# Optimization experiments

Measured on AMD Instinct MI355X. Metric: run time of the kernel, lower is better.

Reference implementation:

```python
import jax, jax.numpy as jnp
import numpy as np
from jax import lax

BATCH = 524288
N_LINKS = 8   # body 0 = fixed base, bodies 1..7 have revolute joints
N_DOFS = 7
G = 9.81      # base linear acceleration z-component encodes gravity

def _skew(v):
    x, y, z = v[..., 0], v[..., 1], v[..., 2]
    o = jnp.zeros_like(x)
    return jnp.stack([jnp.stack([o, -z, y], -1),
                      jnp.stack([z, o, -x], -1),
                      jnp.stack([-y, x, o], -1)], -2)

def _rodrigues(axis, theta):
    # rotation about unit axis by theta; broadcasts axis[...,3] with theta[...]
    K = _skew(axis)
    s = jnp.sin(theta)[..., None, None]
    c = jnp.cos(theta)[..., None, None]
    I = jnp.eye(3, dtype=jnp.result_type(theta))
    return I + s * K + (1.0 - c) * (K @ K)

def setup_inputs():
    key = jax.random.key(0)
    ks = jax.random.split(key, 10)
    q = jax.random.normal(ks[0], (BATCH, N_DOFS), jnp.float32)
    qd = jax.random.normal(ks[1], (BATCH, N_DOFS), jnp.float32)
    qdd_des = jax.random.normal(ks[2], (BATCH, N_DOFS), jnp.float32)
    # fixed (URDF) joint transforms: valid random rotations + link-offset translations
    ax = jax.random.normal(ks[3], (N_LINKS, 3), jnp.float32)
    ax = ax / jnp.linalg.norm(ax, axis=-1, keepdims=True)
    ang = jax.random.uniform(ks[4], (N_LINKS,), jnp.float32, -1.0, 1.0)
    rot_fix = _rodrigues(ax, ang)
    trans_fix = jax.random.uniform(ks[5], (N_LINKS, 3), jnp.float32, -0.25, 0.25)
    # single-coordinate joint axes with signs, as in URDF revolute joints
    joint_axes = jnp.asarray([[0, 0, 1], [0, 1, 0], [0, 0, 1], [0, -1, 0],
                              [0, 0, 1], [0, 1, 0], [0, 0, 1]], jnp.float32)
    mass = jax.random.uniform(ks[6], (N_LINKS,), jnp.float32, 0.5, 4.0)
    com = 0.05 * jax.random.normal(ks[7], (N_LINKS, 3), jnp.float32)
    A = 0.1 * jax.random.normal(ks[8], (N_LINKS, 3, 3), jnp.float32)
    inertia = A @ jnp.swapaxes(A, -1, -2) + 0.05 * jnp.eye(3, dtype=jnp.float32)
    damping = jax.random.uniform(ks[9], (N_DOFS,), jnp.float32, 0.01, 0.2)
    return dict(q=q, qd=qd, qdd_des=qdd_des, rot_fix=rot_fix, trans_fix=trans_fix,
                joint_axes=joint_axes, mass=mass, com=com, inertia=inertia, damping=damping)

def reference(q, qd, qdd_des, rot_fix, trans_fix, joint_axes, mass, com, inertia, damping):
    # Batched recursive Newton-Euler inverse dynamics over a serial chain,
    # matching DifferentiableRobotModel.compute_inverse_dynamics (gravity+damping on).
    B, D = q.shape
    # joint pose of body i(=dof j+1): rotation = rot_fix[i] @ R(axis_j, q_j), translation = trans_fix[i]
    Rq = _rodrigues(joint_axes[None, :, :], q)                     # [B,D,3,3]
    R = jnp.einsum('dij,bdjk->dbik', rot_fix[1:], Rq)              # [D,B,3,3]
    p = trans_fix[1:]                                              # [D,3]
    jv = qd.T[:, :, None] * joint_axes[:, None, :]                 # [D,B,3] joint angular vel
    ja = qdd_des.T[:, :, None] * joint_axes[:, None, :]            # [D,B,3] joint angular acc

    z = jnp.zeros((B, 3), q.dtype)
    base_acc_lin = z.at[:, 2].set(G)

    # forward pass: propagate spatial velocity/acceleration root -> leaf
    def fwd_step(carry, xs):
        vl, va, al, aa = carry
        Ri, pi, jvi, jai = xs
        Rt = jnp.swapaxes(Ri, -1, -2)
        pinv = -jnp.einsum('bij,j->bi', Rt, pi)
        # SpatialMotionVec.transform with inverse joint pose (Rt, pinv)
        va_n = jnp.einsum('bij,bj->bi', Rt, va)
        vl_n = jnp.einsum('bij,bj->bi', Rt, vl) + jnp.cross(pinv, va_n)
        va_i = va_n + jvi
        vl_i = vl_n
        aa_n = jnp.einsum('bij,bj->bi', Rt, aa)
        al_n = jnp.einsum('bij,bj->bi', Rt, al) + jnp.cross(pinv, aa_n)
        # acc = parent_acc(transformed) + joint_acc + vel x joint_vel (joint_vel.lin = 0)
        aa_i = aa_n + jai + jnp.cross(va_i, jvi)
        al_i = al_n + jnp.cross(vl_i, jvi)
        new = (vl_i, va_i, al_i, aa_i)
        return new, new

    _, (vl, va, al, aa) = lax.scan(fwd_step, (z, z, base_acc_lin, z), (R, p, jv, ja))

    # spatial inertia (about body frame origin) acting on motion vectors
    m = mass[1:, None, None]                                       # [D,1,1]
    mc = mass[1:, None] * com[1:]                                  # [D,3]
    cs = _skew(com[1:])
    Io = inertia[1:] + mass[1:, None, None] * (cs @ jnp.swapaxes(cs, -1, -2))

    def imul(lin, ang):
        return (m * lin + jnp.cross(ang, mc[:, None, :]),
                jnp.einsum('dij,dbj->dbi', Io, ang) + jnp.cross(mc[:, None, :], lin))

    Ia_l, Ia_a = imul(al, aa)
    Iv_l, Iv_a = imul(vl, va)
    # f = I*acc + vel x* (I*vel)
    f_l = Ia_l + jnp.cross(va, Iv_l)
    f_a = Ia_a + jnp.cross(va, Iv_a) + jnp.cross(vl, Iv_l)

    # backward pass: accumulate forces leaf -> root; tau_j = f.ang . axis_j
    def bwd_step(carry, xs):
        cl, ca = carry
        fl, fa, Ri, pi, axi = xs
        tl = fl + cl
        ta = fa + ca
        tau = jnp.einsum('bi,i->b', ta, axi)
        # SpatialForceVec.transform with joint pose (Ri, pi)
        nl = jnp.einsum('bij,bj->bi', Ri, tl)
        na = jnp.einsum('bij,bj->bi', Ri, ta) + jnp.cross(pi[None, :], nl)
        return (nl, na), tau

    _, taus = lax.scan(bwd_step, (z, z), (f_l, f_a, R, p, joint_axes), reverse=True)
    return jnp.swapaxes(taus, 0, 1) + damping[None, :] * qd        # [B,D]
```

## Files before the change

kernel.cpp:

```cpp
#include <hip/hip_runtime.h>

#define NDOF 7
#define BLK 256
#define CST_STRIDE 24
#define CST_TOT (NDOF * CST_STRIDE)
#define SF_FLOATS (NDOF * 6 * BLK)

struct V3 { float x, y, z; };
__device__ __forceinline__ V3 operator+(V3 a, V3 b) { return {a.x + b.x, a.y + b.y, a.z + b.z}; }
__device__ __forceinline__ V3 operator-(V3 a, V3 b) { return {a.x - b.x, a.y - b.y, a.z - b.z}; }
__device__ __forceinline__ V3 operator*(float s, V3 a) { return {s * a.x, s * a.y, s * a.z}; }
__device__ __forceinline__ V3 cross(V3 a, V3 b) {
    return {a.y * b.z - a.z * b.y, a.z * b.x - a.x * b.z, a.x * b.y - a.y * b.x};
}
__device__ __forceinline__ float dot(V3 a, V3 b) { return a.x * b.x + a.y * b.y + a.z * b.z; }

template <int AX>
__device__ __forceinline__ void make_R(V3 Fc0, V3 Fc1, V3 Fc2, float s, float c,
                                       V3& R0, V3& R1, V3& R2) {
    if (AX == 0) {
        R0 = c * Fc0 + s * Fc1;
        R1 = c * Fc1 - s * Fc0;
        R2 = Fc2;
    } else if (AX == 1) {
        R0 = c * Fc0 - s * Fc2;
        R1 = Fc1;
        R2 = s * Fc0 + c * Fc2;
    } else {
        R0 = c * Fc0 + s * Fc2;
        R1 = Fc1;
        R2 = c * Fc2 - s * Fc0;
    }
}

template <int AX>
__device__ __forceinline__ void fwd_step(const float4* C4, float s, float c,
                                         float qd, float qdd, V3& vl, V3& va, V3& al,
                                         V3& aa, V3& fl, V3& fa) {
    const float4 A0 = C4[0], A1 = C4[1], A2 = C4[2], A3 = C4[3], A4 = C4[4], A5 = C4[5];
    const V3 Fc0{A0.x, A0.y, A0.z};
    const V3 Fc1{A0.w, A1.x, A1.y};
    const V3 Fc2{A1.z, A1.w, A2.x};
    const V3 p{A2.y, A2.z, A2.w};
    const float I00 = A3.x, I01 = A3.y, I02 = A3.z, I11 = A3.w, I12 = A4.x, I22 = A4.y;
    const float m = A4.z;
    const V3 mc{A4.w, A5.x, A5.y};

    V3 R0, R1, R2;
    make_R<AX>(Fc0, Fc1, Fc2, s, c, R0, R1, R2);

    V3 w1 = vl + cross(va, p);
    V3 w2 = al + cross(aa, p);
    V3 nvl{dot(R0, w1), dot(R1, w1), dot(R2, w1)};
    V3 nva{dot(R0, va), dot(R1, va), dot(R2, va)};
    V3 nal{dot(R0, w2), dot(R1, w2), dot(R2, w2)};
    V3 naa{dot(R0, aa), dot(R1, aa), dot(R2, aa)};

    if (AX == 0) {
        va = {nva.x, nva.y, nva.z + qd};
        aa = {naa.x + va.y * qd, naa.y - va.x * qd, naa.z + qdd};
        vl = nvl;
        al = {nal.x + vl.y * qd, nal.y - vl.x * qd, nal.z};
    } else if (AX == 1) {
        va = {nva.x, nva.y + qd, nva.z};
        aa = {naa.x - va.z * qd, naa.y + qdd, naa.z + va.x * qd};
        vl = nvl;
        al = {nal.x - vl.z * qd, nal.y, nal.z + vl.x * qd};
    } else {
        va = {nva.x, nva.y - qd, nva.z};
        aa = {naa.x + va.z * qd, naa.y - qdd, naa.z - va.x * qd};
        vl = nvl;
        al = {nal.x + vl.z * qd, nal.y, nal.z - vl.x * qd};
    }

    V3 Ial = m * al + cross(aa, mc);
    V3 Iaa = V3{I00 * aa.x + I01 * aa.y + I02 * aa.z,
                I01 * aa.x + I11 * aa.y + I12 * aa.z,
                I02 * aa.x + I12 * aa.y + I22 * aa.z} + cross(mc, al);
    V3 Ivl = m * vl + cross(va, mc);
    V3 Iva = V3{I00 * va.x + I01 * va.y + I02 * va.z,
                I01 * va.x + I11 * va.y + I12 * va.z,
                I02 * va.x + I12 * va.y + I22 * va.z} + cross(mc, vl);
    fl = Ial + cross(va, Ivl);
    fa = Iaa + cross(va, Iva) + cross(vl, Ivl);
}

template <int AX>
__device__ __forceinline__ float bwd_core(const float4* C4, float s, float c,
                                          V3 fl, V3 fa, V3& cl, V3& ca) {
    const float4 A0 = C4[0], A1 = C4[1], A2 = C4[2];
    const V3 Fc0{A0.x, A0.y, A0.z};
    const V3 Fc1{A0.w, A1.x, A1.y};
    const V3 Fc2{A1.z, A1.w, A2.x};
    const V3 p{A2.y, A2.z, A2.w};

    V3 tl = fl + cl;
    V3 ta = fa + ca;
    float tau;
    if (AX == 0) tau = ta.z;
    else if (AX == 1) tau = ta.y;
    else tau = -ta.y;

    V3 R0, R1, R2;
    make_R<AX>(Fc0, Fc1, Fc2, s, c, R0, R1, R2);
    V3 nl = tl.x * R0 + tl.y * R1 + tl.z * R2;
    V3 na = ta.x * R0 + ta.y * R1 + ta.z * R2 + cross(p, nl);
    cl = nl;
    ca = na;
    return tau;
}

__device__ __forceinline__ int axid(int d) { return (d & 1) ? ((d == 3) ? 2 : 1) : 0; }

__global__ __launch_bounds__(BLK) void rnea_main(
    const float* __restrict__ q_g, const float* __restrict__ qd_g,
    const float* __restrict__ qdd_g,
    const float* __restrict__ rot_fix, const float* __restrict__ trans_fix,
    const float* __restrict__ mass_g, const float* __restrict__ com_g,
    const float* __restrict__ inertia_g, const float* __restrict__ damping_g,
    float* __restrict__ out, int nbatch) {
    __shared__ __align__(16) float sC[CST_TOT];
    __shared__ float sF[SF_FLOATS];
    const int t = threadIdx.x;
    const int row = blockIdx.x * BLK + t;
    const bool ok = row < nbatch;
    const int rc = ok ? row : (nbatch - 1);
    const size_t go = (size_t)rc * NDOF;

    if (t < NDOF) {
        const int d = t;
        float* o = sC + d * CST_STRIDE;
        const float* F = rot_fix + (1 + d) * 9;
#pragma unroll
        for (int j = 0; j < 3; j++)
#pragma unroll
            for (int i = 0; i < 3; i++) o[j * 3 + i] = F[i * 3 + j];
#pragma unroll
        for (int i = 0; i < 3; i++) o[9 + i] = trans_fix[(1 + d) * 3 + i];
        const float m = mass_g[1 + d];
        const float c0 = com_g[(1 + d) * 3 + 0];
        const float c1 = com_g[(1 + d) * 3 + 1];
        const float c2 = com_g[(1 + d) * 3 + 2];
        const float* I = inertia_g + (1 + d) * 9;
        o[12] = I[0] + m * (c1 * c1 + c2 * c2);
        o[13] = I[1] - m * c0 * c1;
        o[14] = I[2] - m * c0 * c2;
        o[15] = I[4] + m * (c0 * c0 + c2 * c2);
        o[16] = I[5] - m * c1 * c2;
        o[17] = I[8] + m * (c0 * c0 + c1 * c1);
        o[18] = m;
        o[19] = m * c0;
        o[20] = m * c1;
        o[21] = m * c2;
        o[22] = damping_g[d];
        o[23] = 0.f;
    }
    __syncthreads();

    V3 vl{0.f, 0.f, 0.f}, va{0.f, 0.f, 0.f}, al{0.f, 0.f, 9.81f}, aa{0.f, 0.f, 0.f};
    float q_n = q_g[go], qd_n = qd_g[go], qdd_n = qdd_g[go];
#pragma clang loop unroll(disable)
    for (int d = 0; d < NDOF; ++d) {
        const float qc = q_n, qdc = qd_n, qddc = qdd_n;
        const int dn = (d < NDOF - 1) ? (d + 1) : (NDOF - 1);
        q_n = q_g[go + dn];
        qd_n = qd_g[go + dn];
        qdd_n = qdd_g[go + dn];
        const float s = __sinf(qc), c = __cosf(qc);
        const float4* C4 = reinterpret_cast<const float4*>(sC) + d * 6;
        V3 fl, fa;
        switch (axid(d)) {
            case 0: fwd_step<0>(C4, s, c, qdc, qddc, vl, va, al, aa, fl, fa); break;
            case 1: fwd_step<1>(C4, s, c, qdc, qddc, vl, va, al, aa, fl, fa); break;
            default: fwd_step<2>(C4, s, c, qdc, qddc, vl, va, al, aa, fl, fa); break;
        }
        float* r = sF + d * 6 * BLK + t;
        r[0 * BLK] = fl.x; r[1 * BLK] = fl.y; r[2 * BLK] = fl.z;
        r[3 * BLK] = fa.x; r[4 * BLK] = fa.y; r[5 * BLK] = fa.z;
    }

    V3 cl{0.f, 0.f, 0.f}, ca{0.f, 0.f, 0.f};
#pragma clang loop unroll(disable)
    for (int d = NDOF - 1; d >= 0; --d) {
        const float qc = q_g[go + d];
        const float qdc = qd_g[go + d];
        const float s = __sinf(qc), c = __cosf(qc);
        const float4* C4 = reinterpret_cast<const float4*>(sC) + d * 6;
        const float* r = sF + d * 6 * BLK + t;
        const V3 fl{r[0 * BLK], r[1 * BLK], r[2 * BLK]};
        const V3 fa{r[3 * BLK], r[4 * BLK], r[5 * BLK]};
        float tau;
        switch (axid(d)) {
            case 0: tau = bwd_core<0>(C4, s, c, fl, fa, cl, ca); break;
            case 1: tau = bwd_core<1>(C4, s, c, fl, fa, cl, ca); break;
            default: tau = bwd_core<2>(C4, s, c, fl, fa, cl, ca); break;
        }
        if (ok) out[go + d] = tau + sC[d * CST_STRIDE + 22] * qdc;
    }
}

extern "C" void kernel_launch(void* const* d_in, const int* in_sizes, int n_in,
                              void* d_out, int out_size, void* d_ws, size_t ws_size,
                              hipStream_t stream) {
    const float* q = (const float*)d_in[0];
    const float* qd = (const float*)d_in[1];
    const float* qdd = (const float*)d_in[2];
    const float* rot_fix = (const float*)d_in[3];
    const float* trans_fix = (const float*)d_in[4];
    const float* mass = (const float*)d_in[6];
    const float* com = (const float*)d_in[7];
    const float* inertia = (const float*)d_in[8];
    const float* damping = (const float*)d_in[9];
    float* out = (float*)d_out;

    const int n_elem = in_sizes[0];
    const int B = n_elem / NDOF;
    const int grid = (B + BLK - 1) / BLK;

    rnea_main<<<grid, BLK, 0, stream>>>(q, qd, qdd, rot_fix, trans_fix, mass, com,
                                        inertia, damping, out, B);
}
```

Measured before the change: 126.8 us.

## Keep last two links in registers and shrink shared force parking

The last two joints' forward and backward steps are peeled out of the loops, so their force vectors stay in registers and the shared-memory force buffer shrinks from seven links to five. This lowers the LDS footprint per block, which may allow more blocks per CU. Computed torques are parked in the reused shared slots and written out together at the end rather than as scattered strided stores inside the backward loop. The peeled code raises register pressure, and because each thread still stores 7 strided floats, the output writes may not coalesce any better.

Measured after the change: 125.6 us. About the same (-1.0%).

```diff
diff --git a/kernel.cpp b/kernel.cpp
--- a/kernel.cpp
+++ b/kernel.cpp
@@ -1,10 +1,11 @@
 #include <hip/hip_runtime.h>
 
 #define NDOF 7
+#define NPARK 5
 #define BLK 256
 #define CST_STRIDE 24
 #define CST_TOT (NDOF * CST_STRIDE)
-#define SF_FLOATS (NDOF * 6 * BLK)
+#define SF_FLOATS (NPARK * 6 * BLK)
 
 struct V3 { float x, y, z; };
 __device__ __forceinline__ V3 operator+(V3 a, V3 b) { return {a.x + b.x, a.y + b.y, a.z + b.z}; }
@@ -160,12 +161,11 @@
     V3 vl{0.f, 0.f, 0.f}, va{0.f, 0.f, 0.f}, al{0.f, 0.f, 9.81f}, aa{0.f, 0.f, 0.f};
     float q_n = q_g[go], qd_n = qd_g[go], qdd_n = qdd_g[go];
 #pragma clang loop unroll(disable)
-    for (int d = 0; d < NDOF; ++d) {
+    for (int d = 0; d < NPARK; ++d) {
         const float qc = q_n, qdc = qd_n, qddc = qdd_n;
-        const int dn = (d < NDOF - 1) ? (d + 1) : (NDOF - 1);
-        q_n = q_g[go + dn];
-        qd_n = qd_g[go + dn];
-        qdd_n = qdd_g[go + dn];
+        q_n = q_g[go + d + 1];
+        qd_n = qd_g[go + d + 1];
+        qdd_n = qdd_g[go + d + 1];
         const float s = __sinf(qc), c = __cosf(qc);
         const float4* C4 = reinterpret_cast<const float4*>(sC) + d * 6;
         V3 fl, fa;
@@ -179,14 +179,31 @@
         r[3 * BLK] = fa.x; r[4 * BLK] = fa.y; r[5 * BLK] = fa.z;
     }
 
+    const float q5 = q_n, qd5 = qd_n, qdd5 = qdd_n;
+    const float q6 = q_g[go + 6], qd6 = qd_g[go + 6], qdd6 = qdd_g[go + 6];
+    const float s5 = __sinf(q5), c5 = __cosf(q5);
+    const float s6 = __sinf(q6), c6 = __cosf(q6);
+    V3 fl5, fa5, fl6, fa6;
+    fwd_step<1>(reinterpret_cast<const float4*>(sC) + 5 * 6, s5, c5, qd5, qdd5,
+                vl, va, al, aa, fl5, fa5);
+    fwd_step<0>(reinterpret_cast<const float4*>(sC) + 6 * 6, s6, c6, qd6, qdd6,
+                vl, va, al, aa, fl6, fa6);
+
     V3 cl{0.f, 0.f, 0.f}, ca{0.f, 0.f, 0.f};
+    const float tau6 = bwd_core<0>(reinterpret_cast<const float4*>(sC) + 6 * 6,
+                                   s6, c6, fl6, fa6, cl, ca) +
+                       sC[6 * CST_STRIDE + 22] * qd6;
+    const float tau5 = bwd_core<1>(reinterpret_cast<const float4*>(sC) + 5 * 6,
+                                   s5, c5, fl5, fa5, cl, ca) +
+                       sC[5 * CST_STRIDE + 22] * qd5;
+
 #pragma clang loop unroll(disable)
-    for (int d = NDOF - 1; d >= 0; --d) {
+    for (int d = NPARK - 1; d >= 0; --d) {
         const float qc = q_g[go + d];
         const float qdc = qd_g[go + d];
         const float s = __sinf(qc), c = __cosf(qc);
         const float4* C4 = reinterpret_cast<const float4*>(sC) + d * 6;
-        const float* r = sF + d * 6 * BLK + t;
+        float* r = sF + d * 6 * BLK + t;
         const V3 fl{r[0 * BLK], r[1 * BLK], r[2 * BLK]};
         const V3 fa{r[3 * BLK], r[4 * BLK], r[5 * BLK]};
         float tau;
@@ -195,7 +212,14 @@
             case 1: tau = bwd_core<1>(C4, s, c, fl, fa, cl, ca); break;
             default: tau = bwd_core<2>(C4, s, c, fl, fa, cl, ca); break;
         }
-        if (ok) out[go + d] = tau + sC[d * CST_STRIDE + 22] * qdc;
+        r[0] = tau + sC[d * CST_STRIDE + 22] * qdc;
+    }
+
+    if (ok) {
+#pragma unroll
+        for (int d = 0; d < NPARK; ++d) out[go + d] = sF[d * 6 * BLK + t];
+        out[go + 5] = tau5;
+        out[go + 6] = tau6;
     }
 }
 
```

## Process two rows per thread, fuse last two links, precompute constants in prep kernel

Applied to the files above, without the earlier changes.

Each thread now handles two batch rows with a 128-thread block, so constant loads from shared memory and the switch overhead are shared across both rows. The last two links are fused forward and backward in registers, which removes their shared-memory force parking. The per-link constants are built once by a separate tiny kernel into workspace instead of in every block, and the taus are staged in shared memory before being stored. This raises register pressure and adds a second launch in exchange for better ILP and less shared traffic.

Result: slower. 130.3 us (+2.8%).

```diff
diff --git a/kernel.cpp b/kernel.cpp
--- a/kernel.cpp
+++ b/kernel.cpp
@@ -1,10 +1,12 @@
 #include <hip/hip_runtime.h>
 
 #define NDOF 7
-#define BLK 256
+#define NPARK 5
+#define BLK 128
+#define RPB 256
 #define CST_STRIDE 24
 #define CST_TOT (NDOF * CST_STRIDE)
-#define SF_FLOATS (NDOF * 6 * BLK)
+#define SF_FLOATS (NPARK * 6 * RPB)
 
 struct V3 { float x, y, z; };
 __device__ __forceinline__ V3 operator+(V3 a, V3 b) { return {a.x + b.x, a.y + b.y, a.z + b.z}; }
@@ -14,6 +16,42 @@
     return {a.y * b.z - a.z * b.y, a.z * b.x - a.x * b.z, a.x * b.y - a.y * b.x};
 }
 __device__ __forceinline__ float dot(V3 a, V3 b) { return a.x * b.x + a.y * b.y + a.z * b.z; }
+
+__global__ void rnea_prep(const float* __restrict__ rot_fix,
+                          const float* __restrict__ trans_fix,
+                          const float* __restrict__ mass_g,
+                          const float* __restrict__ com_g,
+                          const float* __restrict__ inertia_g,
+                          const float* __restrict__ damping_g,
+                          float* __restrict__ cst) {
+    const int d = threadIdx.x;
+    if (d >= NDOF) return;
+    float* o = cst + d * CST_STRIDE;
+    const float* F = rot_fix + (1 + d) * 9;
+#pragma unroll
+    for (int j = 0; j < 3; j++)
+#pragma unroll
+        for (int i = 0; i < 3; i++) o[j * 3 + i] = F[i * 3 + j];
+#pragma unroll
+    for (int i = 0; i < 3; i++) o[9 + i] = trans_fix[(1 + d) * 3 + i];
+    const float m = mass_g[1 + d];
+    const float c0 = com_g[(1 + d) * 3 + 0];
+    const float c1 = com_g[(1 + d) * 3 + 1];
+    const float c2 = com_g[(1 + d) * 3 + 2];
+    const float* I = inertia_g + (1 + d) * 9;
+    o[12] = I[0] + m * (c1 * c1 + c2 * c2);
+    o[13] = I[1] - m * c0 * c1;
+    o[14] = I[2] - m * c0 * c2;
+    o[15] = I[4] + m * (c0 * c0 + c2 * c2);
+    o[16] = I[5] - m * c1 * c2;
+    o[17] = I[8] + m * (c0 * c0 + c1 * c1);
+    o[18] = m;
+    o[19] = m * c0;
+    o[20] = m * c1;
+    o[21] = m * c2;
+    o[22] = damping_g[d];
+    o[23] = 0.f;
+}
 
 template <int AX>
 __device__ __forceinline__ void make_R(V3 Fc0, V3 Fc1, V3 Fc2, float s, float c,
@@ -34,10 +72,10 @@
 }
 
 template <int AX>
-__device__ __forceinline__ void fwd_step(const float4* C4, float s, float c,
+__device__ __forceinline__ void fwd_step(float4 A0, float4 A1, float4 A2, float4 A3,
+                                         float4 A4, float4 A5, float s, float c,
                                          float qd, float qdd, V3& vl, V3& va, V3& al,
                                          V3& aa, V3& fl, V3& fa) {
-    const float4 A0 = C4[0], A1 = C4[1], A2 = C4[2], A3 = C4[3], A4 = C4[4], A5 = C4[5];
     const V3 Fc0{A0.x, A0.y, A0.z};
     const V3 Fc1{A0.w, A1.x, A1.y};
     const V3 Fc2{A1.z, A1.w, A2.x};
@@ -86,9 +124,9 @@
 }
 
 template <int AX>
-__device__ __forceinline__ float bwd_core(const float4* C4, float s, float c,
+__device__ __forceinline__ float bwd_core(float4 A0, float4 A1, float4 A2,
+                                          float s, float c,
                                           V3 fl, V3 fa, V3& cl, V3& ca) {
-    const float4 A0 = C4[0], A1 = C4[1], A2 = C4[2];
     const V3 Fc0{A0.x, A0.y, A0.z};
     const V3 Fc1{A0.w, A1.x, A1.y};
     const V3 Fc2{A1.z, A1.w, A2.x};
@@ -114,88 +152,139 @@
 
 __global__ __launch_bounds__(BLK) void rnea_main(
     const float* __restrict__ q_g, const float* __restrict__ qd_g,
-    const float* __restrict__ qdd_g,
-    const float* __restrict__ rot_fix, const float* __restrict__ trans_fix,
-    const float* __restrict__ mass_g, const float* __restrict__ com_g,
-    const float* __restrict__ inertia_g, const float* __restrict__ damping_g,
+    const float* __restrict__ qdd_g, const float* __restrict__ cst,
     float* __restrict__ out, int nbatch) {
     __shared__ __align__(16) float sC[CST_TOT];
     __shared__ float sF[SF_FLOATS];
     const int t = threadIdx.x;
-    const int row = blockIdx.x * BLK + t;
-    const bool ok = row < nbatch;
-    const int rc = ok ? row : (nbatch - 1);
-    const size_t go = (size_t)rc * NDOF;
-
-    if (t < NDOF) {
-        const int d = t;
-        float* o = sC + d * CST_STRIDE;
-        const float* F = rot_fix + (1 + d) * 9;
-#pragma unroll
-        for (int j = 0; j < 3; j++)
-#pragma unroll
-            for (int i = 0; i < 3; i++) o[j * 3 + i] = F[i * 3 + j];
-#pragma unroll
-        for (int i = 0; i < 3; i++) o[9 + i] = trans_fix[(1 + d) * 3 + i];
-        const float m = mass_g[1 + d];
-        const float c0 = com_g[(1 + d) * 3 + 0];
-        const float c1 = com_g[(1 + d) * 3 + 1];
-        const float c2 = com_g[(1 + d) * 3 + 2];
-        const float* I = inertia_g + (1 + d) * 9;
-        o[12] = I[0] + m * (c1 * c1 + c2 * c2);
-        o[13] = I[1] - m * c0 * c1;
-        o[14] = I[2] - m * c0 * c2;
-        o[15] = I[4] + m * (c0 * c0 + c2 * c2);
-        o[16] = I[5] - m * c1 * c2;
-        o[17] = I[8] + m * (c0 * c0 + c1 * c1);
-        o[18] = m;
-        o[19] = m * c0;
-        o[20] = m * c1;
-        o[21] = m * c2;
-        o[22] = damping_g[d];
-        o[23] = 0.f;
-    }
+    const int rowA = blockIdx.x * RPB + t;
+    const int rowB = rowA + BLK;
+    const bool okA = rowA < nbatch;
+    const bool okB = rowB < nbatch;
+    const int rcA = okA ? rowA : (nbatch - 1);
+    const int rcB = okB ? rowB : (nbatch - 1);
+    const size_t goA = (size_t)rcA * NDOF;
+    const size_t goB = (size_t)rcB * NDOF;
+
+    if (t < CST_TOT / 4)
+        reinterpret_cast<float4*>(sC)[t] = reinterpret_cast<const float4*>(cst)[t];
     __syncthreads();
 
-    V3 vl{0.f, 0.f, 0.f}, va{0.f, 0.f, 0.f}, al{0.f, 0.f, 9.81f}, aa{0.f, 0.f, 0.f};
-    float q_n = q_g[go], qd_n = qd_g[go], qdd_n = qdd_g[go];
+    V3 vlA{0.f, 0.f, 0.f}, vaA{0.f, 0.f, 0.f}, alA{0.f, 0.f, 9.81f}, aaA{0.f, 0.f, 0.f};
+    V3 vlB{0.f, 0.f, 0.f}, vaB{0.f, 0.f, 0.f}, alB{0.f, 0.f, 9.81f}, aaB{0.f, 0.f, 0.f};
+    float qAn = q_g[goA], qdAn = qd_g[goA], qddAn = qdd_g[goA];
+    float qBn = q_g[goB], qdBn = qd_g[goB], qddBn = qdd_g[goB];
 #pragma clang loop unroll(disable)
-    for (int d = 0; d < NDOF; ++d) {
-        const float qc = q_n, qdc = qd_n, qddc = qdd_n;
-        const int dn = (d < NDOF - 1) ? (d + 1) : (NDOF - 1);
-        q_n = q_g[go + dn];
-        qd_n = qd_g[go + dn];
-        qdd_n = qdd_g[go + dn];
-        const float s = __sinf(qc), c = __cosf(qc);
+    for (int d = 0; d < NPARK; ++d) {
+        const float qA = qAn, qdA = qdAn, qddA = qddAn;
+        const float qB = qBn, qdB = qdBn, qddB = qddBn;
+        qAn = q_g[goA + d + 1];
+        qdAn = qd_g[goA + d + 1];
+        qddAn = qdd_g[goA + d + 1];
+        qBn = q_g[goB + d + 1];
+        qdBn = qd_g[goB + d + 1];
+        qddBn = qdd_g[goB + d + 1];
+        const float sA = __sinf(qA), cA = __cosf(qA);
+        const float sB = __sinf(qB), cB = __cosf(qB);
         const float4* C4 = reinterpret_cast<const float4*>(sC) + d * 6;
-        V3 fl, fa;
+        const float4 A0 = C4[0], A1 = C4[1], A2 = C4[2], A3 = C4[3], A4 = C4[4], A5 = C4[5];
+        V3 flA, faA, flB, faB;
         switch (axid(d)) {
-            case 0: fwd_step<0>(C4, s, c, qdc, qddc, vl, va, al, aa, fl, fa); break;
-            case 1: fwd_step<1>(C4, s, c, qdc, qddc, vl, va, al, aa, fl, fa); break;
-            default: fwd_step<2>(C4, s, c, qdc, qddc, vl, va, al, aa, fl, fa); break;
+            case 0:
+                fwd_step<0>(A0, A1, A2, A3, A4, A5, sA, cA, qdA, qddA, vlA, vaA, alA, aaA, flA, faA);
+                fwd_step<0>(A0, A1, A2, A3, A4, A5, sB, cB, qdB, qddB, vlB, vaB, alB, aaB, flB, faB);
+                break;
+            case 1:
+                fwd_step<1>(A0, A1, A2, A3, A4, A5, sA, cA, qdA, qddA, vlA, vaA, alA, aaA, flA, faA);
+                fwd_step<1>(A0, A1, A2, A3, A4, A5, sB, cB, qdB, qddB, vlB, vaB, alB, aaB, flB, faB);
+                break;
+            default:
+                fwd_step<2>(A0, A1, A2, A3, A4, A5, sA, cA, qdA, qddA, vlA, vaA, alA, aaA, flA, faA);
+                fwd_step<2>(A0, A1, A2, A3, A4, A5, sB, cB, qdB, qddB, vlB, vaB, alB, aaB, flB, faB);
+                break;
         }
-        float* r = sF + d * 6 * BLK + t;
-        r[0 * BLK] = fl.x; r[1 * BLK] = fl.y; r[2 * BLK] = fl.z;
-        r[3 * BLK] = fa.x; r[4 * BLK] = fa.y; r[5 * BLK] = fa.z;
-    }
-
-    V3 cl{0.f, 0.f, 0.f}, ca{0.f, 0.f, 0.f};
+        float* r = sF + d * 6 * RPB + t;
+        r[0 * RPB] = flA.x; r[1 * RPB] = flA.y; r[2 * RPB] = flA.z;
+        r[3 * RPB] = faA.x; r[4 * RPB] = faA.y; r[5 * RPB] = faA.z;
+        float* r2 = r + BLK;
+        r2[0 * RPB] = flB.x; r2[1 * RPB] = flB.y; r2[2 * RPB] = flB.z;
+        r2[3 * RPB] = faB.x; r2[4 * RPB] = faB.y; r2[5 * RPB] = faB.z;
+    }
+
+    const float q5A = qAn, qd5A = qdAn, qdd5A = qddAn;
+    const float q5B = qBn, qd5B = qdBn, qdd5B = qddBn;
+    const float q6A = q_g[goA + 6], qd6A = qd_g[goA + 6], qdd6A = qdd_g[goA + 6];
+    const float q6B = q_g[goB + 6], qd6B = qd_g[goB + 6], qdd6B = qdd_g[goB + 6];
+    const float s5A = __sinf(q5A), c5A = __cosf(q5A);
+    const float s5B = __sinf(q5B), c5B = __cosf(q5B);
+    const float s6A = __sinf(q6A), c6A = __cosf(q6A);
+    const float s6B = __sinf(q6B), c6B = __cosf(q6B);
+    float tau5A, tau6A, tau5B, tau6B;
+    V3 clA{0.f, 0.f, 0.f}, caA{0.f, 0.f, 0.f};
+    V3 clB{0.f, 0.f, 0.f}, caB{0.f, 0.f, 0.f};
+    {
+        const float4* C5 = reinterpret_cast<const float4*>(sC) + 5 * 6;
+        const float4 B0 = C5[0], B1 = C5[1], B2 = C5[2], B3 = C5[3], B4 = C5[4], B5 = C5[5];
+        const float4* C6 = reinterpret_cast<const float4*>(sC) + 6 * 6;
+        const float4 D0 = C6[0], D1 = C6[1], D2 = C6[2], D3 = C6[3], D4 = C6[4], D5 = C6[5];
+        V3 fl5A, fa5A, fl6A, fa6A, fl5B, fa5B, fl6B, fa6B;
+        fwd_step<1>(B0, B1, B2, B3, B4, B5, s5A, c5A, qd5A, qdd5A, vlA, vaA, alA, aaA, fl5A, fa5A);
+        fwd_step<1>(B0, B1, B2, B3, B4, B5, s5B, c5B, qd5B, qdd5B, vlB, vaB, alB, aaB, fl5B, fa5B);
+        fwd_step<0>(D0, D1, D2, D3, D4, D5, s6A, c6A, qd6A, qdd6A, vlA, vaA, alA, aaA, fl6A, fa6A);
+        fwd_step<0>(D0, D1, D2, D3, D4, D5, s6B, c6B, qd6B, qdd6B, vlB, vaB, alB, aaB, fl6B, fa6B);
+        tau6A = bwd_core<0>(D0, D1, D2, s6A, c6A, fl6A, fa6A, clA, caA) + D5.z * qd6A;
+        tau6B = bwd_core<0>(D0, D1, D2, s6B, c6B, fl6B, fa6B, clB, caB) + D5.z * qd6B;
+        tau5A = bwd_core<1>(B0, B1, B2, s5A, c5A, fl5A, fa5A, clA, caA) + B5.z * qd5A;
+        tau5B = bwd_core<1>(B0, B1, B2, s5B, c5B, fl5B, fa5B, clB, caB) + B5.z * qd5B;
+    }
+
 #pragma clang loop unroll(disable)
-    for (int d = NDOF - 1; d >= 0; --d) {
-        const float qc = q_g[go + d];
-        const float qdc = qd_g[go + d];
-        const float s = __sinf(qc), c = __cosf(qc);
+    for (int d = NPARK - 1; d >= 0; --d) {
+        const float qA = q_g[goA + d];
+        const float qdA = qd_g[goA + d];
+        const float qB = q_g[goB + d];
+        const float qdB = qd_g[goB + d];
+        const float sA = __sinf(qA), cA = __cosf(qA);
+        const float sB = __sinf(qB), cB = __cosf(qB);
         const float4* C4 = reinterpret_cast<const float4*>(sC) + d * 6;
-        const float* r = sF + d * 6 * BLK + t;
-        const V3 fl{r[0 * BLK], r[1 * BLK], r[2 * BLK]};
-        const V3 fa{r[3 * BLK], r[4 * BLK], r[5 * BLK]};
-        float tau;
+        const float4 A0 = C4[0], A1 = C4[1], A2 = C4[2];
+        const float damp = sC[d * CST_STRIDE + 22];
+        float* r = sF + d * 6 * RPB + t;
+        const V3 flA{r[0 * RPB], r[1 * RPB], r[2 * RPB]};
+        const V3 faA{r[3 * RPB], r[4 * RPB], r[5 * RPB]};
+        float* r2 = r + BLK;
+        const V3 flB{r2[0 * RPB], r2[1 * RPB], r2[2 * RPB]};
+        const V3 faB{r2[3 * RPB], r2[4 * RPB], r2[5 * RPB]};
+        float tauA, tauB;
         switch (axid(d)) {
-            case 0: tau = bwd_core<0>(C4, s, c, fl, fa, cl, ca); break;
-            case 1: tau = bwd_core<1>(C4, s, c, fl, fa, cl, ca); break;
-            default: tau = bwd_core<2>(C4, s, c, fl, fa, cl, ca); break;
+            case 0:
+                tauA = bwd_core<0>(A0, A1, A2, sA, cA, flA, faA, clA, caA);
+                tauB = bwd_core<0>(A0, A1, A2, sB, cB, flB, faB, clB, caB);
+                break;
+            case 1:
+                tauA = bwd_core<1>(A0, A1, A2, sA, cA, flA, faA, clA, caA);
+                tauB = bwd_core<1>(A0, A1, A2, sB, cB, flB, faB, clB, caB);
+                break;
+            default:
+                tauA = bwd_core<2>(A0, A1, A2, sA, cA, flA, faA, clA, caA);
+                tauB = bwd_core<2>(A0, A1, A2, sB, cB, flB, faB, clB, caB);
+                break;
         }
-        if (ok) out[go + d] = tau + sC[d * CST_STRIDE + 22] * qdc;
+        r[0] = tauA + damp * qdA;
+        r2[0] = tauB + damp * qdB;
+    }
+
+    if (okA) {
+#pragma unroll
+        for (int d = 0; d < NPARK; ++d) out[goA + d] = sF[d * 6 * RPB + t];
+        out[goA + 5] = tau5A;
+        out[goA + 6] = tau6A;
+    }
+    if (okB) {
+#pragma unroll
+        for (int d = 0; d < NPARK; ++d) out[goB + d] = sF[d * 6 * RPB + t + BLK];
+        out[goB + 5] = tau5B;
+        out[goB + 6] = tau6B;
     }
 }
 
@@ -212,11 +301,12 @@
     const float* inertia = (const float*)d_in[8];
     const float* damping = (const float*)d_in[9];
     float* out = (float*)d_out;
+    float* cst = (float*)d_ws;
 
     const int n_elem = in_sizes[0];
     const int B = n_elem / NDOF;
-    const int grid = (B + BLK - 1) / BLK;
-
-    rnea_main<<<grid, BLK, 0, stream>>>(q, qd, qdd, rot_fix, trans_fix, mass, com,
-                                        inertia, damping, out, B);
-}
+    const int grid = (B + RPB - 1) / RPB;
+
+    rnea_prep<<<1, 64, 0, stream>>>(rot_fix, trans_fix, mass, com, inertia, damping, cst);
+    rnea_main<<<grid, BLK, 0, stream>>>(q, qd, qdd, cst, out, B);
+}
```
